# Performance work log

Measured on AMD Instinct MI355X. Metric: run time of the kernel, lower is better.

Reference implementation:

```python
import jax, jax.numpy as jnp
import numpy as np

B, N, DIM = 4, 4096, 512
HEADS, DHEAD, CHUNK = 4, 128, 64
MAX_LR = 1.0
EPS = 1e-6


def rmsnorm(x):
    return x * jax.lax.rsqrt(jnp.mean(x * x, axis=-1, keepdims=True) + EPS)


def mem_mlp(params, x):
    # MemoryMLP depth=2: x @ W1 -> silu -> @ W2 (no biases)
    W1, W2 = params
    return jax.nn.silu(x @ W1) @ W2


def assoc_scan(gates, x):
    # linear recurrence y_i = g_i * y_{i-1} + x_i along axis=1 (chunks)
    def op(a, b):
        ga, xa = a
        gb, xb = b
        return (ga * gb, gb * xa + xb)
    _, y = jax.lax.associative_scan(op, (gates, x), axis=1)
    return y


def setup_inputs() -> dict:
    key = jax.random.key(0)
    ks = jax.random.split(key, 12)
    di = HEADS * DHEAD
    nrm = lambda k, shp, sc: jax.random.normal(k, shp, jnp.float32) * sc
    return {
        'seq': nrm(ks[0], (B, N, DIM), 1.0),
        'g_store': jnp.ones((DIM,), jnp.float32),
        'g_retrieve': jnp.ones((DIM,), jnp.float32),
        'W_q': nrm(ks[1], (DIM, di), DIM ** -0.5),
        'W_kv': nrm(ks[2], (DIM, 2 * di), DIM ** -0.5),
        'W_step': nrm(ks[3], (DIM, HEADS), DIM ** -0.5),
        'W_mom': nrm(ks[4], (DIM, HEADS), DIM ** -0.5),
        'W_decay': nrm(ks[5], (DIM, HEADS), DIM ** -0.5),
        'W_gate': nrm(ks[6], (DIM, HEADS), DIM ** -0.5),
        'gamma_mh': jnp.zeros((HEADS, 1, DHEAD), jnp.float32),
        'W_o': nrm(ks[7], (di, DIM), di ** -0.5),
        'M_W1': nrm(ks[8], (DHEAD, DHEAD), DHEAD ** -0.5),
        'M_W2': nrm(ks[9], (DHEAD, DHEAD), DHEAD ** -0.5),
    }


def reference(seq, g_store, g_retrieve, W_q, W_kv, W_step, W_mom, W_decay,
              W_gate, gamma_mh, W_o, M_W1, M_W2):
    b, n, dim = seq.shape
    h, d, c = HEADS, DHEAD, CHUNK
    nc = n // c
    bh = b * h

    # ---------------- store path ----------------
    s = rmsnorm(seq) * g_store                                   # (b,n,dim)
    lr = jax.nn.sigmoid(s @ W_step) * MAX_LR                     # (b,n,h)
    lr_c = lr.transpose(0, 2, 1).reshape(bh, nc, c)              # (bh,nc,c)
    chunked = s.reshape(b, nc, c, dim).mean(2)                   # (b,nc,dim)
    decay = jax.nn.sigmoid(chunked @ W_decay).transpose(0, 2, 1).reshape(bh, nc)
    mom = jax.nn.sigmoid(chunked @ W_mom).transpose(0, 2, 1).reshape(bh, nc)

    kv = s @ W_kv                                                # (b,n,2*h*d)
    k, v = jnp.split(kv, 2, axis=-1)
    to_chunks = lambda t: t.reshape(b, n, h, d).transpose(0, 2, 1, 3).reshape(bh, nc, c, d)
    k, v = to_chunks(k), to_chunks(v)

    # per-chunk gradient at the initial memory weights (vmap(grad))
    def chunk_loss(params, kc, lrc, vc):
        pred = mem_mlp(params, kc)                               # (c,d)
        loss = jnp.mean((pred - vc) ** 2, axis=-1)               # (c,)
        return jnp.sum(loss * lrc)

    gfn = jax.vmap(jax.vmap(jax.grad(chunk_loss),
                            in_axes=((None, None), 0, 0, 0)),
                   in_axes=((None, None), 0, 0, 0))
    g1, g2 = gfn((M_W1, M_W2), k, lr_c, v)                       # (bh,nc,d,d)
    s1, s2 = -g1, -g2                                            # surprises

    # momentum assoc scan: m_i = mom_i * m_{i-1} + s_i
    momg = mom[:, :, None, None]
    m1 = assoc_scan(momg, s1)
    m2 = assoc_scan(momg, s2)

    # decay-gated weight recurrence with prev = initial weights:
    # W_i = (1 - decay_i) * W_{i-1} + m_i,  W_0 = init
    def scan_with_init(gates, x, w0):
        g = jnp.concatenate([jnp.ones_like(gates[:, :1]), gates], axis=1)
        x0 = jnp.broadcast_to(w0, (bh, 1) + w0.shape)
        return assoc_scan(g, jnp.concatenate([x0, x], axis=1))   # (bh,nc+1,d,d)

    dg = (1.0 - decay)[:, :, None, None]
    u1 = scan_with_init(dg, m1, M_W1)
    u2 = scan_with_init(dg, m2, M_W2)
    # retrieval for chunk i uses weights after chunk i-1 (paper semantics)
    w1c, w2c = u1[:, :-1], u2[:, :-1]                            # (bh,nc,d,d)

    # ---------------- retrieve path ----------------
    r = rmsnorm(seq) * g_retrieve
    q = to_chunks(r @ W_q)                                       # (bh,nc,c,d)
    pred = jax.vmap(jax.vmap(lambda w1, w2, qc: mem_mlp((w1, w2), qc)))(w1c, w2c, q)
    out = pred.reshape(b, h, n, d)
    out = rmsnorm(out) * (gamma_mh + 1.0)                        # multihead rmsnorm
    gate = jax.nn.sigmoid(r @ W_gate)                            # (b,n,h)
    out = out * gate.transpose(0, 2, 1)[..., None]               # retrieve gate
    out = out.transpose(0, 2, 1, 3).reshape(b, n, h * d)         # merge heads
    return out @ W_o                                             # combine heads
```

## Files before the change

kernel.cpp:

```cpp
#include <hip/hip_runtime.h>

typedef unsigned short u16;
typedef unsigned int u32;
typedef __attribute__((ext_vector_type(8))) short s16x8;
typedef __attribute__((ext_vector_type(4))) float f32x4;

#define DEV __device__ __forceinline__
#define MFMA16(a,b,c) __builtin_amdgcn_mfma_f32_16x16x32_bf16(a,b,c,0,0,0)

DEV float bf2f(u16 x){ u32 u=((u32)x)<<16; float f; __builtin_memcpy(&f,&u,4); return f; }
DEV u16 f2bf(float f){ u32 u; __builtin_memcpy(&u,&f,4); u32 r=u+0x7FFFu+((u>>16)&1u); return (u16)(r>>16); }
DEV uint4 pack8(const float* f){
  uint4 v;
  v.x=(u32)f2bf(f[0])|((u32)f2bf(f[1])<<16);
  v.y=(u32)f2bf(f[2])|((u32)f2bf(f[3])<<16);
  v.z=(u32)f2bf(f[4])|((u32)f2bf(f[5])<<16);
  v.w=(u32)f2bf(f[6])|((u32)f2bf(f[7])<<16);
  return v;
}
DEV float sigm(float x){ return 1.0f/(1.0f+__expf(-x)); }


DEV void trans_tile_a(const float* src, u16* dst, int K, int Nn, int bx, int by,
                      int tid, bool act, float* ld )
{
  int n0 = bx*64, k0 = by*64;
  if (act){
    #pragma unroll
    for (int rr=0; rr<4; rr++){
      int kk = rr*16 + (tid>>4);
      int nn = (tid&15)*4;
      float4 v = *(const float4*)(src + (size_t)(k0+kk)*Nn + n0 + nn);
      ld[kk*65+nn]=v.x; ld[kk*65+nn+1]=v.y; ld[kk*65+nn+2]=v.z; ld[kk*65+nn+3]=v.w;
    }
  }
  __syncthreads();
  if (act){
    int nn2 = tid>>2, kb = (tid&3)*16;
    float o[16];
    #pragma unroll
    for (int j=0;j<16;j++) o[j] = ld[(kb+j)*65+nn2];
    u16* dp = dst + (size_t)(n0+nn2)*K + k0 + kb;
    *(uint4*)dp     = pack8(&o[0]);
    *(uint4*)(dp+8) = pack8(&o[8]);
  }
}

__global__ __launch_bounds__(512) void k_front(const float* __restrict__ seq,
    const float* __restrict__ gs, const float* __restrict__ gr,
    const float* __restrict__ Wstep, const float* __restrict__ Wgate,
    const float* __restrict__ Wdec, const float* __restrict__ Wmom,
    const float* __restrict__ Wkv, const float* __restrict__ Wq,
    const float* __restrict__ Wo, const float* __restrict__ MW1,
    const float* __restrict__ MW2,
    u16* __restrict__ s, u16* __restrict__ r,
    float* __restrict__ lr, float* __restrict__ gate,
    float* __restrict__ momv, float* __restrict__ dgv,
    u16* __restrict__ Wkvt, u16* __restrict__ Wqt, u16* __restrict__ Wot,
    u16* __restrict__ W1t, u16* __restrict__ W2t, u16* __restrict__ W2s)
{
  __shared__ float smem[8192];
  const int blk = blockIdx.x;
  const int tid = threadIdx.x;

  if (blk >= 256){
    int l = blk - 256;
    bool act = tid < 256;
    int t2 = tid & 255;
    if (l < 128)      trans_tile_a(Wkv, Wkvt, 512, 1024, l&15, l>>4, t2, act, smem);
    else if (l < 192){ int m = l-128; trans_tile_a(Wq, Wqt, 512, 512, m&7, m>>3, t2, act, smem); }
    else if (l < 256){ int m = l-192; trans_tile_a(Wo, Wot, 512, 512, m&7, m>>3, t2, act, smem); }
    else if (l < 260){ int m = l-256; trans_tile_a(MW1, W1t, 128, 128, m&1, m>>1, t2, act, smem); }
    else if (l < 264){ int m = l-260; trans_tile_a(MW2, W2t, 128, 128, m&1, m>>1, t2, act, smem); }
    else {
      __syncthreads();
      if (act){
        int e = ((l-264)*256 + t2)*8;
        float f[8];
        *(float4*)&f[0] = *(const float4*)(MW2+e);
        *(float4*)&f[4] = *(const float4*)(MW2+e+4);
        *(uint4*)(W2s+e) = pack8(f);
      }
    }
    return;
  }

  float* pchunk = smem;
  float* red    = smem + 4096;
  const int b = blk >> 6, ci = blk & 63;
  const int wv = tid >> 6, lane = tid & 63;
  const size_t rowbase = (size_t)b*4096 + (size_t)ci*64;

  float psum[8] = {0,0,0,0,0,0,0,0};
  #pragma unroll 1
  for (int tt=0; tt<8; tt++){
    int t = wv*8 + tt;
    const float* row = seq + (rowbase + t)*512;
    float x[8];
    *(float4*)&x[0] = *(const float4*)(row + lane*8);
    *(float4*)&x[4] = *(const float4*)(row + lane*8 + 4);
    float ss = 0.f;
    #pragma unroll
    for (int j=0;j<8;j++) ss += x[j]*x[j];
    #pragma unroll
    for (int o=32;o>=1;o>>=1) ss += __shfl_xor(ss, o, 64);
    float inv = rsqrtf(ss*(1.0f/512.0f) + 1e-6f);
    float al[4] = {0,0,0,0}, ag[4] = {0,0,0,0};
    float sv8[8], rv8[8];
    #pragma unroll
    for (int j=0;j<8;j++){
      int d = lane*8 + j;
      float sn = x[j]*inv;
      float sv = sn*gs[d];
      float rv = sn*gr[d];
      sv8[j]=sv; rv8[j]=rv;
      psum[j] += sv;
      float4 wst = *(const float4*)(Wstep + d*4);
      float4 wgt = *(const float4*)(Wgate + d*4);
      al[0]+=sv*wst.x; al[1]+=sv*wst.y; al[2]+=sv*wst.z; al[3]+=sv*wst.w;
      ag[0]+=rv*wgt.x; ag[1]+=rv*wgt.y; ag[2]+=rv*wgt.z; ag[3]+=rv*wgt.w;
    }
    *(uint4*)(s + (rowbase+t)*512 + lane*8) = pack8(sv8);
    *(uint4*)(r + (rowbase+t)*512 + lane*8) = pack8(rv8);
    #pragma unroll
    for (int o=32;o>=1;o>>=1){
      #pragma unroll
      for (int h=0;h<4;h++){ al[h] += __shfl_xor(al[h], o, 64); ag[h] += __shfl_xor(ag[h], o, 64); }
    }
    if (lane == 0){
      #pragma unroll
      for (int h=0;h<4;h++){
        lr[(rowbase+t)*4 + h]   = sigm(al[h]);
        gate[(rowbase+t)*4 + h] = sigm(ag[h]);
      }
    }
  }
  #pragma unroll
  for (int j=0;j<8;j++) pchunk[wv*512 + lane*8+j] = psum[j];
  __syncthreads();
  {
    int d = tid;
    float mean = 0.f;
    #pragma unroll
    for (int w=0;w<8;w++) mean += pchunk[w*512 + d];
    mean *= (1.0f/64.0f);
    #pragma unroll
    for (int h=0;h<4;h++){
      red[h*512 + d]     = mean*Wdec[d*4+h];
      red[(4+h)*512 + d] = mean*Wmom[d*4+h];
    }
  }
  __syncthreads();
  {
    float sum = 0.f;
    #pragma unroll
    for (int j=0;j<8;j++) sum += red[wv*512 + lane*8+j];
    #pragma unroll
    for (int o=32;o>=1;o>>=1) sum += __shfl_xor(sum, o, 64);
    if (lane == 0){
      if (wv < 4) dgv[((size_t)(b*4+wv))*64 + ci]      = 1.0f - sigm(sum);
      else        momv[((size_t)(b*4+(wv-4)))*64 + ci] = sigm(sum);
    }
  }
}

template<bool OUT_BF>
DEV void gemm_body(const u16* A, const u16* Bt, void* Cv, int K, int ldc,
                   int bx, int by, u16* sA, u16* sB)
{
  const int tid = threadIdx.x;
  const int wv = tid>>6, lane = tid&63, lrow = lane&15, lk = lane>>4;
  const int wm = (wv>>1)*64, wn = (wv&1)*64;
  const int rowbase = by*128, colbase = bx*128;
  const int srow = lane>>3;
  const int scol = (lane&7)*8;
  f32x4 acc[4][4] = {};
  for (int kc = 0; kc < K; kc += 64){
    __syncthreads();
    #pragma unroll
    for (int it=0; it<4; ++it){
      int seg = it*4 + wv;
      int row = seg*8 + srow;
      __builtin_amdgcn_global_load_lds(
        (const __attribute__((address_space(1))) void*)(A + (size_t)(rowbase+row)*K + kc + scol),
        (__attribute__((address_space(3))) void*)&sA[seg*512 + lane*8], 16, 0, 0);
      __builtin_amdgcn_global_load_lds(
        (const __attribute__((address_space(1))) void*)(Bt + (size_t)(colbase+row)*K + kc + scol),
        (__attribute__((address_space(3))) void*)&sB[seg*512 + lane*8], 16, 0, 0);
    }
    __syncthreads();
    #pragma unroll
    for (int k0=0;k0<2;k0++){
      s16x8 a[4], b[4];
      #pragma unroll
      for (int m=0;m<4;m++) a[m] = *(const s16x8*)&sA[(wm+m*16+lrow)*64 + k0*32 + lk*8];
      #pragma unroll
      for (int n=0;n<4;n++) b[n] = *(const s16x8*)&sB[(wn+n*16+lrow)*64 + k0*32 + lk*8];
      #pragma unroll
      for (int m=0;m<4;m++)
        #pragma unroll
        for (int n=0;n<4;n++)
          acc[m][n] = MFMA16(a[m], b[n], acc[m][n]);
    }
  }
  #pragma unroll
  for (int m=0;m<4;m++)
    #pragma unroll
    for (int n=0;n<4;n++)
      #pragma unroll
      for (int r=0;r<4;r++){
        int row = rowbase + wm + m*16 + lk*4 + r;
        int col = colbase + wn + n*16 + lrow;
        float v = acc[m][n][r];
        if (OUT_BF) ((u16*)Cv)[(size_t)row*ldc + col] = f2bf(v);
        else        ((float*)Cv)[(size_t)row*ldc + col] = v;
      }
}

__global__ __launch_bounds__(256) void k_gemmAB(const u16* __restrict__ A1,
    const u16* __restrict__ B1, u16* __restrict__ C1,
    const u16* __restrict__ A2, const u16* __restrict__ B2, u16* __restrict__ C2)
{
  __shared__ u16 sA[128*64];
  __shared__ u16 sB[128*64];
  int bid = blockIdx.x;
  if (bid < 1024){
    int s = (bid & 7)*128 + (bid >> 3);
    gemm_body<true>(A1, B1, C1, 512, 1024, s & 7, s >> 3, sA, sB);
  } else {
    int l = bid - 1024;
    int s = (l & 7)*64 + (l >> 3);
    gemm_body<true>(A2, B2, C2, 512, 512, s & 3, s >> 2, sA, sB);
  }
}

template<bool OUT_BF>
__global__ __launch_bounds__(256) void k_gemm1(const u16* __restrict__ A,
    const u16* __restrict__ Bt, void* __restrict__ Cv, int K, int ldc, int nbx, int cpx)
{
  __shared__ u16 sA[128*64];
  __shared__ u16 sB[128*64];
  int bid = blockIdx.x;
  int s = (bid & 7)*cpx + (bid >> 3);
  gemm_body<OUT_BF>(A, Bt, Cv, K, ldc, s % nbx, s / nbx, sA, sB);
}

__global__ __launch_bounds__(256,4) void k_grad(const u16* __restrict__ kv,
    const float* __restrict__ lr, const u16* __restrict__ W1t,
    const u16* __restrict__ W2t, const u16* __restrict__ W2s,
    u16* __restrict__ s1, u16* __restrict__ s2)
{
  __shared__ u16 bufR[64*136];
  __shared__ u16 bufAt[128*68];
  __shared__ u16 bufPt[128*68];
  __shared__ float lrs[64];

  const int blk = blockIdx.x;
  const int bhi = blk >> 6, ci = blk & 63;
  const int b = bhi >> 2, hd = bhi & 3;
  const int tid = threadIdx.x;
  const int wv = tid>>6, lane = tid&63, lrow = lane&15, lk = lane>>4;
  int col[2]; col[0] = wv*32 + lrow; col[1] = wv*32 + 16 + lrow;
  const int f_hi[2] = { (lrow>>3)*128, ((16+lrow)>>3)*128 };
  const int f_lo[2] = { lrow&7, (16+lrow)&7 };
  const int fbase = wv*512;
  const size_t rowbase = (size_t)b*4096 + (size_t)ci*64;
  const u16* kvb = kv + rowbase*1024 + hd*128;

  #pragma unroll
  for (int rep=0;rep<4;rep++){
    int lin = rep*2048 + tid*8;
    int i = lin >> 7, d = lin & 127;
    *(uint4*)&bufR[i*136 + d] = *(const uint4*)(kvb + (size_t)i*1024 + d);
  }
  if (tid < 64) lrs[tid] = lr[(rowbase + tid)*4 + hd] * (2.0f/128.0f);
  __syncthreads();

  float spv[4][2][4];

  {
    f32x4 acc[4][2] = {};
    #pragma unroll
    for (int k0=0;k0<4;k0++){
      s16x8 w0 = *(const s16x8*)(W1t + col[0]*128 + k0*32 + lk*8);
      s16x8 w1 = *(const s16x8*)(W1t + col[1]*128 + k0*32 + lk*8);
      #pragma unroll
      for (int m=0;m<4;m++){
        s16x8 a = *(const s16x8*)&bufR[(m*16+lrow)*136 + k0*32 + lk*8];
        acc[m][0] = MFMA16(a, w0, acc[m][0]);
        acc[m][1] = MFMA16(a, w1, acc[m][1]);
      }
    }
    __syncthreads();
    #pragma unroll
    for (int m=0;m<4;m++)
      #pragma unroll
      for (int n=0;n<2;n++){
        int row0 = m*16 + lk*4;
        u16 av4[4];
        #pragma unroll
        for (int r=0;r<4;r++){
          float h = acc[m][n][r];
          float sg = sigm(h);
          av4[r] = f2bf(h*sg);
          spv[m][n][r] = sg*(1.0f + h*(1.0f - sg));
          bufR[(row0+r)*136 + col[n]] = av4[r];
        }
        *(uint2*)&bufAt[col[n]*68 + row0] = make_uint2(
          (u32)av4[0] | ((u32)av4[1]<<16), (u32)av4[2] | ((u32)av4[3]<<16));
      }
  }
  __syncthreads();

  {
    f32x4 acc[4][2] = {};
    #pragma unroll
    for (int k0=0;k0<4;k0++){
      s16x8 w0 = *(const s16x8*)(W2t + col[0]*128 + k0*32 + lk*8);
      s16x8 w1 = *(const s16x8*)(W2t + col[1]*128 + k0*32 + lk*8);
      #pragma unroll
      for (int m=0;m<4;m++){
        s16x8 a = *(const s16x8*)&bufR[(m*16+lrow)*136 + k0*32 + lk*8];
        acc[m][0] = MFMA16(a, w0, acc[m][0]);
        acc[m][1] = MFMA16(a, w1, acc[m][1]);
      }
    }
    u16 vv[4][2][4];
    #pragma unroll
    for (int m=0;m<4;m++)
      #pragma unroll
      for (int n=0;n<2;n++)
        #pragma unroll
        for (int r=0;r<4;r++)
          vv[m][n][r] = kvb[(size_t)(m*16+lk*4+r)*1024 + 512 + col[n]];
    __syncthreads();
    #pragma unroll
    for (int m=0;m<4;m++)
      #pragma unroll
      for (int n=0;n<2;n++){
        int row0 = m*16 + lk*4;
        u16 dp4[4];
        #pragma unroll
        for (int r=0;r<4;r++){
          float dp = lrs[row0+r]*(acc[m][n][r] - bf2f(vv[m][n][r]));
          dp4[r] = f2bf(dp);
          bufR[(row0+r)*136 + col[n]] = dp4[r];
        }
        *(uint2*)&bufPt[col[n]*68 + row0] = make_uint2(
          (u32)dp4[0] | ((u32)dp4[1]<<16), (u32)dp4[2] | ((u32)dp4[3]<<16));
      }
  }
  __syncthreads();

  {
    f32x4 da[4][2] = {};
    #pragma unroll
    for (int k0=0;k0<4;k0++){
      s16x8 w0 = *(const s16x8*)(W2s + col[0]*128 + k0*32 + lk*8);
      s16x8 w1 = *(const s16x8*)(W2s + col[1]*128 + k0*32 + lk*8);
      #pragma unroll
      for (int m=0;m<4;m++){
        s16x8 a = *(const s16x8*)&bufR[(m*16+lrow)*136 + k0*32 + lk*8];
        da[m][0] = MFMA16(a, w0, da[m][0]);
        da[m][1] = MFMA16(a, w1, da[m][1]);
      }
    }
    __syncthreads();
    #pragma unroll
    for (int m=0;m<4;m++)
      #pragma unroll
      for (int n=0;n<2;n++){
        int row0 = m*16 + lk*4;
        u16 dh4[4];
        #pragma unroll
        for (int r=0;r<4;r++) dh4[r] = f2bf(spv[m][n][r]*da[m][n][r]);
        *(uint2*)&bufR[col[n]*68 + row0] = make_uint2(
          (u32)dh4[0] | ((u32)dh4[1]<<16), (u32)dh4[2] | ((u32)dh4[3]<<16));
      }
  }

  const size_t outbase = (size_t)blk * 16384;

  s16x8 kbf[2][2];
  #pragma unroll
  for (int n=0;n<2;n++)
    #pragma unroll
    for (int k0=0;k0<2;k0++)
      #pragma unroll
      for (int j=0;j<8;j++)
        ((u16*)&kbf[n][k0])[j] = kvb[(size_t)(k0*32 + lk*8 + j)*1024 + col[n]];
  {
    f32x4 acc[8][2] = {};
    #pragma unroll
    for (int k0=0;k0<2;k0++){
      s16x8 bf0 = *(const s16x8*)&bufAt[col[0]*68 + k0*32 + lk*8];
      s16x8 bf1 = *(const s16x8*)&bufAt[col[1]*68 + k0*32 + lk*8];
      #pragma unroll
      for (int m=0;m<8;m++){
        s16x8 a = *(const s16x8*)&bufPt[(m*16+lrow)*68 + k0*32 + lk*8];
        acc[m][0] = MFMA16(a, bf0, acc[m][0]);
        acc[m][1] = MFMA16(a, bf1, acc[m][1]);
      }
    }
    #pragma unroll
    for (int m=0;m<8;m++)
      #pragma unroll
      for (int n=0;n<2;n++)
        #pragma unroll
        for (int r=0;r<4;r++)
          s2[outbase + m*2048 + fbase + f_hi[n] + (lk*4+r)*8 + f_lo[n]] = f2bf(-acc[m][n][r]);
  }
  __syncthreads();

  {
    f32x4 acc[8][2] = {};
    #pragma unroll
    for (int k0=0;k0<2;k0++)
      #pragma unroll
      for (int m=0;m<8;m++){
        s16x8 a = *(const s16x8*)&bufR[(m*16+lrow)*68 + k0*32 + lk*8];
        acc[m][0] = MFMA16(a, kbf[0][k0], acc[m][0]);
        acc[m][1] = MFMA16(a, kbf[1][k0], acc[m][1]);
      }
    #pragma unroll
    for (int m=0;m<8;m++)
      #pragma unroll
      for (int n=0;n<2;n++)
        #pragma unroll
        for (int r=0;r<4;r++)
          s1[outbase + m*2048 + fbase + f_hi[n] + (lk*4+r)*8 + f_lo[n]] = f2bf(-acc[m][n][r]);
  }
}

__global__ __launch_bounds__(256) void k_scan(const float* __restrict__ momv,
    const float* __restrict__ dgv, const float* __restrict__ MW1,
    const float* __restrict__ MW2, u16* __restrict__ s1w, u16* __restrict__ s2w)
{
  int bhi = blockIdx.x >> 5, eb = blockIdx.x & 31;
  int e0 = eb*512 + threadIdx.x*2;
  int colD = ((e0>>11)<<4) + ((e0>>3)&15);
  int kD   = ((e0>>9)&3)*32 + ((e0>>7)&3)*8 + (e0&7);
  float u1a = MW1[kD*128 + colD];
  float u1b = MW1[(kD+1)*128 + colD];
  float u2a = MW2[kD*128 + colD];
  float u2b = MW2[(kD+1)*128 + colD];
  float m1a = 0.f, m1b = 0.f, m2a = 0.f, m2b = 0.f;
  size_t base = (size_t)bhi*64*16384 + e0;
  const float* mv = momv + bhi*64;
  const float* dv = dgv + bhi*64;
  #pragma unroll 4
  for (int t=0; t<64; t++){
    float g  = mv[t];
    float dg = dv[t];
    size_t idx = base + (size_t)t*16384;
    u32 a = *(const u32*)(s1w + idx);
    u32 c = *(const u32*)(s2w + idx);
    *(u32*)(s1w + idx) = (u32)f2bf(u1a) | ((u32)f2bf(u1b)<<16);
    *(u32*)(s2w + idx) = (u32)f2bf(u2a) | ((u32)f2bf(u2b)<<16);
    m1a = g*m1a + bf2f((u16)(a&0xffffu));
    m1b = g*m1b + bf2f((u16)(a>>16));
    m2a = g*m2a + bf2f((u16)(c&0xffffu));
    m2b = g*m2b + bf2f((u16)(c>>16));
    u1a = dg*u1a + m1a;
    u1b = dg*u1b + m1b;
    u2a = dg*u2a + m2a;
    u2b = dg*u2b + m2b;
  }
}

__global__ __launch_bounds__(512) void k_retr(const u16* __restrict__ qin,
    const u16* __restrict__ w1c, const u16* __restrict__ w2c,
    const float* __restrict__ gate, const float* __restrict__ gamma,
    u16* __restrict__ outp)
{
  __shared__ u16 bufQ[64*136];
  __shared__ u16 bufA[64*132];
  __shared__ float rsum[8][64];
  const int blk = blockIdx.x;
  const int bhi = blk >> 6, ci = blk & 63;
  const int b = bhi >> 2, hd = bhi & 3;
  const int tid = threadIdx.x;
  const int wv = tid>>6, lane = tid&63, lrow = lane&15, lk = lane>>4;
  const int colw = wv*16 + lrow;
  const size_t rowbase = (size_t)b*4096 + (size_t)ci*64;
  const u16* w1 = w1c + (size_t)blk*16384;
  const u16* w2 = w2c + (size_t)blk*16384;
  const int lane8 = lane*8;

  #pragma unroll
  for (int rep=0;rep<2;rep++){
    int lin = rep*4096 + tid*8;
    int i = lin>>7, d = lin&127;
    *(uint4*)&bufQ[i*136 + d] = *(const uint4*)(qin + (rowbase+i)*512 + hd*128 + d);
  }
  __syncthreads();

  {
    s16x8 wf[4];
    #pragma unroll
    for (int k0=0;k0<4;k0++) wf[k0] = *(const s16x8*)(w1 + wv*2048 + k0*512 + lane8);
    f32x4 acc[4] = {};
    #pragma unroll
    for (int k0=0;k0<4;k0++){
      #pragma unroll
      for (int m=0;m<4;m++){
        s16x8 a = *(const s16x8*)&bufQ[(m*16+lrow)*136 + k0*32 + lk*8];
        acc[m] = MFMA16(a, wf[k0], acc[m]);
      }
    }
    #pragma unroll
    for (int m=0;m<4;m++){
      #pragma unroll
      for (int r=0;r<4;r++){
        float h = acc[m][r];
        bufA[(m*16+lk*4+r)*132 + colw] = f2bf(h*sigm(h));
      }
    }
  }
  __syncthreads();

  f32x4 acc[4] = {};
  {
    s16x8 wf[4];
    #pragma unroll
    for (int k0=0;k0<4;k0++) wf[k0] = *(const s16x8*)(w2 + wv*2048 + k0*512 + lane8);
    #pragma unroll
    for (int k0=0;k0<4;k0++){
      #pragma unroll
      for (int m=0;m<4;m++){
        s16x8 a = *(const s16x8*)&bufA[(m*16+lrow)*132 + k0*32 + lk*8];
        acc[m] = MFMA16(a, wf[k0], acc[m]);
      }
    }
  }
  #pragma unroll
  for (int m=0;m<4;m++){
    #pragma unroll
    for (int r=0;r<4;r++){
      float p = acc[m][r]*acc[m][r];
      p += __shfl_xor(p, 1, 64);
      p += __shfl_xor(p, 2, 64);
      p += __shfl_xor(p, 4, 64);
      p += __shfl_xor(p, 8, 64);
      if (lrow == 0) rsum[wv][m*16 + lk*4 + r] = p;
    }
  }
  __syncthreads();
  float gm = gamma[hd*128 + colw] + 1.0f;
  #pragma unroll
  for (int m=0;m<4;m++){
    #pragma unroll
    for (int r=0;r<4;r++){
      int row = m*16 + lk*4 + r;
      float sum = rsum[0][row]+rsum[1][row]+rsum[2][row]+rsum[3][row]
                + rsum[4][row]+rsum[5][row]+rsum[6][row]+rsum[7][row];
      float inv = rsqrtf(sum*(1.0f/128.0f) + 1e-6f);
      float gt = gate[(rowbase+row)*4 + hd];
      outp[(rowbase+row)*512 + hd*128 + colw] = f2bf(acc[m][r]*inv*gm*gt);
    }
  }
}

extern "C" void kernel_launch(void* const* d_in, const int* in_sizes, int n_in,
                              void* d_out, int out_size, void* d_ws, size_t ws_size,
                              hipStream_t stream)
{
  const float* seq    = (const float*)d_in[0];
  const float* gstore = (const float*)d_in[1];
  const float* gret   = (const float*)d_in[2];
  const float* W_q    = (const float*)d_in[3];
  const float* W_kv   = (const float*)d_in[4];
  const float* W_step = (const float*)d_in[5];
  const float* W_mom  = (const float*)d_in[6];
  const float* W_dec  = (const float*)d_in[7];
  const float* W_gate = (const float*)d_in[8];
  const float* gamma  = (const float*)d_in[9];
  const float* W_o    = (const float*)d_in[10];
  const float* MW1    = (const float*)d_in[11];
  const float* MW2    = (const float*)d_in[12];
  float* out = (float*)d_out;

  const size_t NS = (size_t)16384*512;
  const size_t NG = (size_t)16*64*16384;
  size_t need = (5*NS + 2*NG + 524288 + 262144 + 262144 + 3*16384)*2
              + (2*65536 + 2048)*4;
  if (ws_size < need) return;

  char* ws = (char*)d_ws;
  u16* s_bf = (u16*)ws; ws += NS*2;
  u16* r_bf = (u16*)ws; ws += NS*2;
  u16* kv_bf= (u16*)ws; ws += 2*NS*2;
  u16* q_bf = (u16*)ws; ws += NS*2;
  u16* s1   = (u16*)ws; ws += NG*2;
  u16* s2   = (u16*)ws; ws += NG*2;
  u16* Wkvt = (u16*)ws; ws += (size_t)524288*2;
  u16* Wqt  = (u16*)ws; ws += (size_t)262144*2;
  u16* Wot  = (u16*)ws; ws += (size_t)262144*2;
  u16* W1tb = (u16*)ws; ws += (size_t)16384*2;
  u16* W2tb = (u16*)ws; ws += (size_t)16384*2;
  u16* W2sb = (u16*)ws; ws += (size_t)16384*2;
  float* lr   = (float*)ws; ws += (size_t)65536*4;
  float* gatep= (float*)ws; ws += (size_t)65536*4;
  float* momv = (float*)ws; ws += 1024*4;
  float* dgv  = (float*)ws; ws += 1024*4;
  u16* outp = s_bf;

  k_front<<<528, 512, 0, stream>>>(seq, gstore, gret, W_step, W_gate, W_dec, W_mom,
                                   W_kv, W_q, W_o, MW1, MW2,
                                   s_bf, r_bf, lr, gatep, momv, dgv,
                                   Wkvt, Wqt, Wot, W1tb, W2tb, W2sb);
  k_gemmAB<<<1536, 256, 0, stream>>>(s_bf, Wkvt, kv_bf, r_bf, Wqt, q_bf);
  k_grad<<<1024, 256, 0, stream>>>(kv_bf, lr, W1tb, W2tb, W2sb, s1, s2);
  k_scan<<<512, 256, 0, stream>>>(momv, dgv, MW1, MW2, s1, s2);
  k_retr<<<1024, 512, 0, stream>>>(q_bf, s1, s2, gatep, gamma, outp);
  k_gemm1<false><<<512, 256, 0, stream>>>(outp, Wot, out, 512, 512, 4, 64);
}
```

Before: 171.5 us.

## Fuse KV and Q projections into grad and retrieve kernels; widen scan per thread

Removes the standalone KV/Q GEMM kernel. Each k_grad block now computes its own 64x256 slice of k and v from the normalized sequence and the transposed W_kv, and each k_retr block computes its own q tile, so the results stay in LDS instead of going through global memory. The scan kernel now handles four elements per thread with 8-byte accesses and half as many blocks. This saves one launch and the kv/q round trip. In exchange, k_grad and k_retr do extra work and take extra barriers while staging K chunks, and the scan runs with less parallelism.

Result: slower. 202.6 us (+18.2%).

```diff
diff --git a/kernel.cpp b/kernel.cpp
--- a/kernel.cpp
+++ b/kernel.cpp
@@ -22,7 +22,7 @@
 
 
 DEV void trans_tile_a(const float* src, u16* dst, int K, int Nn, int bx, int by,
-                      int tid, bool act, float* ld )
+                      int tid, bool act, float* ld)
 {
   int n0 = bx*64, k0 = by*64;
   if (act){
@@ -217,23 +217,6 @@
       }
 }
 
-__global__ __launch_bounds__(256) void k_gemmAB(const u16* __restrict__ A1,
-    const u16* __restrict__ B1, u16* __restrict__ C1,
-    const u16* __restrict__ A2, const u16* __restrict__ B2, u16* __restrict__ C2)
-{
-  __shared__ u16 sA[128*64];
-  __shared__ u16 sB[128*64];
-  int bid = blockIdx.x;
-  if (bid < 1024){
-    int s = (bid & 7)*128 + (bid >> 3);
-    gemm_body<true>(A1, B1, C1, 512, 1024, s & 7, s >> 3, sA, sB);
-  } else {
-    int l = bid - 1024;
-    int s = (l & 7)*64 + (l >> 3);
-    gemm_body<true>(A2, B2, C2, 512, 512, s & 3, s >> 2, sA, sB);
-  }
-}
-
 template<bool OUT_BF>
 __global__ __launch_bounds__(256) void k_gemm1(const u16* __restrict__ A,
     const u16* __restrict__ Bt, void* __restrict__ Cv, int K, int ldc, int nbx, int cpx)
@@ -245,10 +228,10 @@
   gemm_body<OUT_BF>(A, Bt, Cv, K, ldc, s % nbx, s / nbx, sA, sB);
 }
 
-__global__ __launch_bounds__(256,4) void k_grad(const u16* __restrict__ kv,
-    const float* __restrict__ lr, const u16* __restrict__ W1t,
-    const u16* __restrict__ W2t, const u16* __restrict__ W2s,
-    u16* __restrict__ s1, u16* __restrict__ s2)
+__global__ __launch_bounds__(256,4) void k_grad(const u16* __restrict__ sgl,
+    const u16* __restrict__ Wkvt, const float* __restrict__ lr,
+    const u16* __restrict__ W1t, const u16* __restrict__ W2t,
+    const u16* __restrict__ W2s, u16* __restrict__ s1, u16* __restrict__ s2)
 {
   __shared__ u16 bufR[64*136];
   __shared__ u16 bufAt[128*68];
@@ -265,16 +248,55 @@
   const int f_lo[2] = { lrow&7, (16+lrow)&7 };
   const int fbase = wv*512;
   const size_t rowbase = (size_t)b*4096 + (size_t)ci*64;
-  const u16* kvb = kv + rowbase*1024 + hd*128;
-
+
+  {
+    const int colb = (wv < 2) ? (hd*128 + wv*64) : (512 + hd*128 + (wv-2)*64);
+    f32x4 acc[4][4] = {};
+    #pragma unroll 1
+    for (int cc=0; cc<4; cc++){
+      if (cc) __syncthreads();
+      #pragma unroll
+      for (int rep=0;rep<4;rep++){
+        int lin = rep*2048 + tid*8;
+        int i = lin >> 7, d = lin & 127;
+        *(uint4*)&bufAt[i*136 + d] = *(const uint4*)(sgl + (rowbase+i)*512 + cc*128 + d);
+      }
+      __syncthreads();
+      #pragma unroll
+      for (int k0=0;k0<4;k0++){
+        s16x8 wf[4];
+        #pragma unroll
+        for (int n=0;n<4;n++)
+          wf[n] = *(const s16x8*)(Wkvt + (size_t)(colb + n*16 + lrow)*512 + cc*128 + k0*32 + lk*8);
+        #pragma unroll
+        for (int m=0;m<4;m++){
+          s16x8 a = *(const s16x8*)&bufAt[(m*16+lrow)*136 + k0*32 + lk*8];
+          #pragma unroll
+          for (int n=0;n<4;n++) acc[m][n] = MFMA16(a, wf[n], acc[m][n]);
+        }
+      }
+    }
+    u16* dstb = (wv < 2) ? bufR : bufPt;
+    const int wvb = (wv & 1)*64;
+    #pragma unroll
+    for (int m=0;m<4;m++)
+      #pragma unroll
+      for (int n=0;n<4;n++)
+        #pragma unroll
+        for (int r=0;r<4;r++)
+          dstb[(m*16+lk*4+r)*136 + wvb + n*16 + lrow] = f2bf(acc[m][n][r]);
+  }
+  if (tid < 64) lrs[tid] = lr[(rowbase + tid)*4 + hd] * (2.0f/128.0f);
+  __syncthreads();
+
+  s16x8 kbf[2][2];
   #pragma unroll
-  for (int rep=0;rep<4;rep++){
-    int lin = rep*2048 + tid*8;
-    int i = lin >> 7, d = lin & 127;
-    *(uint4*)&bufR[i*136 + d] = *(const uint4*)(kvb + (size_t)i*1024 + d);
-  }
-  if (tid < 64) lrs[tid] = lr[(rowbase + tid)*4 + hd] * (2.0f/128.0f);
-  __syncthreads();
+  for (int n=0;n<2;n++)
+    #pragma unroll
+    for (int k0=0;k0<2;k0++)
+      #pragma unroll
+      for (int j=0;j<8;j++)
+        ((u16*)&kbf[n][k0])[j] = bufR[(k0*32 + lk*8 + j)*136 + col[n]];
 
   float spv[4][2][4];
 
@@ -332,7 +354,7 @@
       for (int n=0;n<2;n++)
         #pragma unroll
         for (int r=0;r<4;r++)
-          vv[m][n][r] = kvb[(size_t)(m*16+lk*4+r)*1024 + 512 + col[n]];
+          vv[m][n][r] = bufPt[(m*16+lk*4+r)*136 + col[n]];
     __syncthreads();
     #pragma unroll
     for (int m=0;m<4;m++)
@@ -381,14 +403,6 @@
 
   const size_t outbase = (size_t)blk * 16384;
 
-  s16x8 kbf[2][2];
-  #pragma unroll
-  for (int n=0;n<2;n++)
-    #pragma unroll
-    for (int k0=0;k0<2;k0++)
-      #pragma unroll
-      for (int j=0;j<8;j++)
-        ((u16*)&kbf[n][k0])[j] = kvb[(size_t)(k0*32 + lk*8 + j)*1024 + col[n]];
   {
     f32x4 acc[8][2] = {};
     #pragma unroll
@@ -436,15 +450,16 @@
     const float* __restrict__ dgv, const float* __restrict__ MW1,
     const float* __restrict__ MW2, u16* __restrict__ s1w, u16* __restrict__ s2w)
 {
-  int bhi = blockIdx.x >> 5, eb = blockIdx.x & 31;
-  int e0 = eb*512 + threadIdx.x*2;
+  int bhi = blockIdx.x >> 4, eb = blockIdx.x & 15;
+  int e0 = eb*1024 + threadIdx.x*4;
   int colD = ((e0>>11)<<4) + ((e0>>3)&15);
   int kD   = ((e0>>9)&3)*32 + ((e0>>7)&3)*8 + (e0&7);
-  float u1a = MW1[kD*128 + colD];
-  float u1b = MW1[(kD+1)*128 + colD];
-  float u2a = MW2[kD*128 + colD];
-  float u2b = MW2[(kD+1)*128 + colD];
-  float m1a = 0.f, m1b = 0.f, m2a = 0.f, m2b = 0.f;
+  float u1[4], u2[4], m1[4]={0,0,0,0}, m2[4]={0,0,0,0};
+  #pragma unroll
+  for (int j=0;j<4;j++){
+    u1[j] = MW1[(kD+j)*128 + colD];
+    u2[j] = MW2[(kD+j)*128 + colD];
+  }
   size_t base = (size_t)bhi*64*16384 + e0;
   const float* mv = momv + bhi*64;
   const float* dv = dgv + bhi*64;
@@ -453,25 +468,31 @@
     float g  = mv[t];
     float dg = dv[t];
     size_t idx = base + (size_t)t*16384;
-    u32 a = *(const u32*)(s1w + idx);
-    u32 c = *(const u32*)(s2w + idx);
-    *(u32*)(s1w + idx) = (u32)f2bf(u1a) | ((u32)f2bf(u1b)<<16);
-    *(u32*)(s2w + idx) = (u32)f2bf(u2a) | ((u32)f2bf(u2b)<<16);
-    m1a = g*m1a + bf2f((u16)(a&0xffffu));
-    m1b = g*m1b + bf2f((u16)(a>>16));
-    m2a = g*m2a + bf2f((u16)(c&0xffffu));
-    m2b = g*m2b + bf2f((u16)(c>>16));
-    u1a = dg*u1a + m1a;
-    u1b = dg*u1b + m1b;
-    u2a = dg*u2a + m2a;
-    u2b = dg*u2b + m2b;
-  }
-}
-
-__global__ __launch_bounds__(512) void k_retr(const u16* __restrict__ qin,
-    const u16* __restrict__ w1c, const u16* __restrict__ w2c,
-    const float* __restrict__ gate, const float* __restrict__ gamma,
-    u16* __restrict__ outp)
+    uint2 a = *(const uint2*)(s1w + idx);
+    uint2 c = *(const uint2*)(s2w + idx);
+    uint2 w1o, w2o;
+    w1o.x = (u32)f2bf(u1[0]) | ((u32)f2bf(u1[1])<<16);
+    w1o.y = (u32)f2bf(u1[2]) | ((u32)f2bf(u1[3])<<16);
+    w2o.x = (u32)f2bf(u2[0]) | ((u32)f2bf(u2[1])<<16);
+    w2o.y = (u32)f2bf(u2[2]) | ((u32)f2bf(u2[3])<<16);
+    *(uint2*)(s1w + idx) = w1o;
+    *(uint2*)(s2w + idx) = w2o;
+    u16 ah[4] = {(u16)(a.x&0xffffu),(u16)(a.x>>16),(u16)(a.y&0xffffu),(u16)(a.y>>16)};
+    u16 ch[4] = {(u16)(c.x&0xffffu),(u16)(c.x>>16),(u16)(c.y&0xffffu),(u16)(c.y>>16)};
+    #pragma unroll
+    for (int j=0;j<4;j++){
+      m1[j] = g*m1[j] + bf2f(ah[j]);
+      m2[j] = g*m2[j] + bf2f(ch[j]);
+      u1[j] = dg*u1[j] + m1[j];
+      u2[j] = dg*u2[j] + m2[j];
+    }
+  }
+}
+
+__global__ __launch_bounds__(512) void k_retr(const u16* __restrict__ rgl,
+    const u16* __restrict__ Wqt, const u16* __restrict__ w1c,
+    const u16* __restrict__ w2c, const float* __restrict__ gate,
+    const float* __restrict__ gamma, u16* __restrict__ outp)
 {
   __shared__ u16 bufQ[64*136];
   __shared__ u16 bufA[64*132];
@@ -487,11 +508,35 @@
   const u16* w2 = w2c + (size_t)blk*16384;
   const int lane8 = lane*8;
 
-  #pragma unroll
-  for (int rep=0;rep<2;rep++){
-    int lin = rep*4096 + tid*8;
-    int i = lin>>7, d = lin&127;
-    *(uint4*)&bufQ[i*136 + d] = *(const uint4*)(qin + (rowbase+i)*512 + hd*128 + d);
+  {
+    const u16* wq = Wqt + (size_t)(hd*128 + colw)*512;
+    f32x4 qa[4] = {};
+    #pragma unroll 1
+    for (int cc=0; cc<4; cc++){
+      if (cc) __syncthreads();
+      #pragma unroll
+      for (int rep=0;rep<2;rep++){
+        int lin = rep*4096 + tid*8;
+        int i = lin >> 7, d = lin & 127;
+        *(uint4*)&bufQ[i*136 + d] = *(const uint4*)(rgl + (rowbase+i)*512 + cc*128 + d);
+      }
+      __syncthreads();
+      #pragma unroll
+      for (int k0=0;k0<4;k0++){
+        s16x8 wf = *(const s16x8*)(wq + cc*128 + k0*32 + lk*8);
+        #pragma unroll
+        for (int m=0;m<4;m++){
+          s16x8 a = *(const s16x8*)&bufQ[(m*16+lrow)*136 + k0*32 + lk*8];
+          qa[m] = MFMA16(a, wf, qa[m]);
+        }
+      }
+    }
+    __syncthreads();
+    #pragma unroll
+    for (int m=0;m<4;m++)
+      #pragma unroll
+      for (int r=0;r<4;r++)
+        bufQ[(m*16+lk*4+r)*136 + colw] = f2bf(qa[m][r]);
   }
   __syncthreads();
 
@@ -603,15 +648,15 @@
   float* gatep= (float*)ws; ws += (size_t)65536*4;
   float* momv = (float*)ws; ws += 1024*4;
   float* dgv  = (float*)ws; ws += 1024*4;
+  (void)kv_bf; (void)q_bf;
   u16* outp = s_bf;
 
   k_front<<<528, 512, 0, stream>>>(seq, gstore, gret, W_step, W_gate, W_dec, W_mom,
                                    W_kv, W_q, W_o, MW1, MW2,
                                    s_bf, r_bf, lr, gatep, momv, dgv,
                                    Wkvt, Wqt, Wot, W1tb, W2tb, W2sb);
-  k_gemmAB<<<1536, 256, 0, stream>>>(s_bf, Wkvt, kv_bf, r_bf, Wqt, q_bf);
-  k_grad<<<1024, 256, 0, stream>>>(kv_bf, lr, W1tb, W2tb, W2sb, s1, s2);
-  k_scan<<<512, 256, 0, stream>>>(momv, dgv, MW1, MW2, s1, s2);
-  k_retr<<<1024, 512, 0, stream>>>(q_bf, s1, s2, gatep, gamma, outp);
+  k_grad<<<1024, 256, 0, stream>>>(s_bf, Wkvt, lr, W1tb, W2tb, W2sb, s1, s2);
+  k_scan<<<256, 256, 0, stream>>>(momv, dgv, MW1, MW2, s1, s2);
+  k_retr<<<1024, 512, 0, stream>>>(r_bf, Wqt, s1, s2, gatep, gamma, outp);
   k_gemm1<false><<<512, 256, 0, stream>>>(outp, Wot, out, 512, 512, 4, 64);
 }
```
